# Optimization experiments

Hardware: AMD Instinct MI355X
Metric: run time of the kernel (lower is better)

## Reference

```python
import jax, jax.numpy as jnp
import numpy as np
import math

B, C, L = 8, 64, 2048
H = 4            # num_heads
CH = C // H      # head channels = 16
G = max(1, C // 16)  # GroupNorm groups = 4
EPS = 1e-5


def setup_inputs() -> dict:
    key = jax.random.key(0)
    ks = jax.random.split(key, 4)
    x = jax.random.normal(ks[0], (B, C, L), dtype=jnp.float32)
    gn_w = jnp.ones((C,), jnp.float32)
    gn_b = jnp.zeros((C,), jnp.float32)
    qkv_w = jax.random.normal(ks[1], (3 * C, C), jnp.float32) / math.sqrt(C)
    qkv_b = jnp.zeros((3 * C,), jnp.float32)
    # note: original zero-inits proj_out; we use random weights for a non-trivial baseline
    proj_w = jax.random.normal(ks[2], (C, C), jnp.float32) / math.sqrt(C)
    proj_b = jnp.zeros((C,), jnp.float32)
    return {"x": x, "gn_w": gn_w, "gn_b": gn_b, "qkv_w": qkv_w,
            "qkv_b": qkv_b, "proj_w": proj_w, "proj_b": proj_b}


def _group_norm(x, w, b):
    # x: [B, C, L], groups over channel dim
    xg = x.reshape(B, G, (C // G) * L)
    mean = jnp.mean(xg, axis=-1, keepdims=True)
    var = jnp.var(xg, axis=-1, keepdims=True)
    xn = ((xg - mean) * jax.lax.rsqrt(var + EPS)).reshape(B, C, L)
    return xn * w[None, :, None] + b[None, :, None]


def reference(x, gn_w, gn_b, qkv_w, qkv_b, proj_w, proj_b):
    xn = _group_norm(x, gn_w, gn_b)
    # conv1x1 QKV: [B, 3C, L]
    qkv = jnp.einsum('oc,bcl->bol', qkv_w, xn) + qkv_b[None, :, None]
    q, k, v = jnp.split(qkv, 3, axis=1)            # each [B, C, L]
    q = q.reshape(B * H, CH, L)
    k = k.reshape(B * H, CH, L)
    v = v.reshape(B * H, CH, L)
    scale = 1.0 / math.sqrt(math.sqrt(CH))          # double-scaled as in source
    w = jnp.einsum('bct,bcs->bts', q * scale, k * scale)  # [B*H, L, L]
    w = jax.nn.softmax(w.astype(jnp.float32), axis=-1).astype(q.dtype)
    a = jnp.einsum('bts,bcs->bct', w, v).reshape(B, C, L)
    h = jnp.einsum('oc,bcl->bol', proj_w, a) + proj_b[None, :, None]
    return x + h
```

## Files before the change

kernel.cpp:

```cpp
#include <hip/hip_runtime.h>
#include <hip/hip_bf16.h>

#define LL 2048

typedef float f32x16 __attribute__((ext_vector_type(16)));
typedef float f32x4 __attribute__((ext_vector_type(4)));
typedef short short8 __attribute__((ext_vector_type(8)));

__device__ __forceinline__ float exp2_fast(float x) {
    float r;
    asm volatile("v_exp_f32 %0, %1" : "=v"(r) : "v"(x));
    return r;
}

__device__ __forceinline__ float rcp_fast(float x) {
    float r;
    asm("v_rcp_f32 %0, %1" : "=v"(r) : "v"(x));
    return r;
}

__device__ __forceinline__ uint32_t cvtpk(float lo, float hi) {
    uint32_t r;
    asm("v_cvt_pk_bf16_f32 %0, %1, %2" : "=v"(r) : "v"(lo), "v"(hi));
    return r;
}

__device__ __forceinline__ unsigned short bf16lo(float a) {
    return (unsigned short)(cvtpk(a, a) & 0xFFFFu);
}

__device__ __forceinline__ void permswap(uint32_t& d, uint32_t& s) {
    asm("v_permlane32_swap_b32 %0, %1" : "+v"(d), "+v"(s));
}

__global__ __launch_bounds__(256) void k_gnstats(const float* __restrict__ x,
                                                 const float* __restrict__ qw,
                                                 const float* __restrict__ pw,
                                                 float* __restrict__ stats,
                                                 unsigned short* __restrict__ ones,
                                                 unsigned short* __restrict__ wqb) {
    if (blockIdx.x == 0) {
        uint4 v = make_uint4(0x3F803F80u, 0x3F803F80u, 0x3F803F80u, 0x3F803F80u);
        *(uint4*)(ones + threadIdx.x * 16)     = v;
        *(uint4*)(ones + threadIdx.x * 16 + 8) = v;
    }
    if (blockIdx.x >= 8 && blockIdx.x < 16) {
        int idx8 = (blockIdx.x - 8) * 2048 + threadIdx.x * 8;
        const float* src = (idx8 < 12288) ? qw + idx8 : pw + (idx8 - 12288);
        f32x4 a = *(const f32x4*)src;
        f32x4 c = *(const f32x4*)(src + 4);
        uint4 o = make_uint4(cvtpk(a[0], a[1]), cvtpk(a[2], a[3]),
                             cvtpk(c[0], c[1]), cvtpk(c[2], c[3]));
        *(uint4*)(wqb + idx8) = o;
    }
    int bg = blockIdx.x >> 2, part = blockIdx.x & 3;
    const f32x4* p = (const f32x4*)(x + (size_t)bg * (16 * LL)) + part * 2048;
    float s1 = 0.f, s2 = 0.f;
    for (int i = threadIdx.x; i < 2048; i += 256) {
        f32x4 v = p[i];
        s1 += v[0] + v[1] + v[2] + v[3];
        s2 += v[0] * v[0] + v[1] * v[1] + v[2] * v[2] + v[3] * v[3];
    }
#pragma unroll
    for (int off = 32; off > 0; off >>= 1) {
        s1 += __shfl_down(s1, off, 64);
        s2 += __shfl_down(s2, off, 64);
    }
    __shared__ float r1[4], r2[4];
    int lane = threadIdx.x & 63, wv = threadIdx.x >> 6;
    if (lane == 0) { r1[wv] = s1; r2[wv] = s2; }
    __syncthreads();
    if (threadIdx.x == 0) {
        stats[blockIdx.x * 2]     = r1[0] + r1[1] + r1[2] + r1[3];
        stats[blockIdx.x * 2 + 1] = r2[0] + r2[1] + r2[2] + r2[3];
    }
}

__global__ __launch_bounds__(256) void k_qkv(const float* __restrict__ x,
                                             const float* __restrict__ gnw,
                                             const float* __restrict__ gnb,
                                             const unsigned short* __restrict__ wqb,
                                             const float* __restrict__ qb,
                                             const float* __restrict__ stats,
                                             unsigned short* __restrict__ qt,
                                             unsigned short* __restrict__ kt,
                                             unsigned short* __restrict__ vb) {
    int lt = blockIdx.x;
    int b  = blockIdx.y;
    int tid = threadIdx.x;
    int l0 = lt * 64;
    __shared__ unsigned short xs[64 * 64];
    __shared__ unsigned short ws[3][64 * 64];
    __shared__ float wb[64][2];

    if (tid < 64) {
        int c = tid, g = c >> 4;
        int sb = (b * 4 + g) * 8;
        float s1 = stats[sb] + stats[sb + 2] + stats[sb + 4] + stats[sb + 6];
        float s2 = stats[sb + 1] + stats[sb + 3] + stats[sb + 5] + stats[sb + 7];
        float mean = s1 * (1.0f / 32768.0f);
        float var  = s2 * (1.0f / 32768.0f) - mean * mean;
        float rstd = rsqrtf(var + 1e-5f);
        float wgt = gnw[c] * rstd;
        wb[c][0] = wgt;
        wb[c][1] = gnb[c] - mean * wgt;
    }
#pragma unroll
    for (int ot = 0; ot < 3; ot++) {
#pragma unroll
        for (int k = 0; k < 4; k++) {
            int chunk = tid + k * 256;
            int o = chunk >> 4, c4 = chunk & 15;
            uint2 w2 = *(const uint2*)(wqb + (size_t)(ot * 64 + o) * 64 + c4 * 4);
            *(uint2*)&ws[ot][o * 64 + ((c4 * 4) ^ ((o & 7) << 3))] = w2;
        }
    }
    __syncthreads();

    {
        int cq = tid >> 4, l4 = tid & 15, c0 = cq * 4;
        f32x4 xv0 = *(const f32x4*)(x + ((size_t)b * 64 + c0)     * LL + l0 + l4 * 4);
        f32x4 xv1 = *(const f32x4*)(x + ((size_t)b * 64 + c0 + 1) * LL + l0 + l4 * 4);
        f32x4 xv2 = *(const f32x4*)(x + ((size_t)b * 64 + c0 + 2) * LL + l0 + l4 * 4);
        f32x4 xv3 = *(const f32x4*)(x + ((size_t)b * 64 + c0 + 3) * LL + l0 + l4 * 4);
        float w0 = wb[c0][0], b0 = wb[c0][1];
        float w1 = wb[c0 + 1][0], b1 = wb[c0 + 1][1];
        float w2 = wb[c0 + 2][0], b2 = wb[c0 + 2][1];
        float w3 = wb[c0 + 3][0], b3 = wb[c0 + 3][1];
#pragma unroll
        for (int j = 0; j < 4; j++) {
            int l = l4 * 4 + j;
            uint32_t lo = cvtpk(xv0[j] * w0 + b0, xv1[j] * w1 + b1);
            uint32_t hw = cvtpk(xv2[j] * w2 + b2, xv3[j] * w3 + b3);
            *(uint2*)&xs[l * 64 + (c0 ^ ((l & 7) << 3))] = make_uint2(lo, hw);
        }
    }
    __syncthreads();

    int wv_ = tid >> 6, lane = tid & 63, hi = lane >> 5, tl = lane & 31;
    int o0 = (wv_ & 1) * 32, lw = (wv_ >> 1) * 32;
    int arow = o0 + tl, brow = lw + tl;
    int t = l0 + lw + tl;

#pragma unroll
    for (int ot = 0; ot < 3; ot++) {
        f32x16 acc = {};
#pragma unroll
        for (int kk = 0; kk < 4; kk++) {
            int cb = kk * 16 + hi * 8;
            short8 af = *(const short8*)&ws[ot][arow * 64 + (cb ^ ((arow & 7) << 3))];
            short8 bf = *(const short8*)&xs[brow * 64 + (cb ^ ((brow & 7) << 3))];
            acc = __builtin_amdgcn_mfma_f32_32x32x16_bf16(af, bf, acc, 0, 0, 0);
        }
        if (ot < 2) {
            float sc = ot ? 0.72134752f : 0.5f;
            unsigned short* base = (ot ? kt : qt) + (size_t)(b * 4) * (LL * 16);
#pragma unroll
            for (int g = 0; g < 4; g++) {
                int ob = o0 + 8 * g + 4 * hi;
                float v0 = (acc[4 * g]     + qb[ot * 64 + ob])     * sc;
                float v1 = (acc[4 * g + 1] + qb[ot * 64 + ob + 1]) * sc;
                float v2 = (acc[4 * g + 2] + qb[ot * 64 + ob + 2]) * sc;
                float v3 = (acc[4 * g + 3] + qb[ot * 64 + ob + 3]) * sc;
                uint2 pkv = make_uint2(cvtpk(v0, v1), cvtpk(v2, v3));
                *(uint2*)(base + (size_t)(ob >> 4) * (LL * 16)
                          + (size_t)t * 16 + (ob & 15)) = pkv;
            }
        } else {
            unsigned short* base = vb + (size_t)(b * 4) * (16 * LL);
#pragma unroll
            for (int r = 0; r < 16; r++) {
                int o = o0 + (r & 3) + 8 * (r >> 2) + 4 * hi;
                base[(size_t)(o >> 4) * (16 * LL) + (size_t)(o & 15) * LL + t] =
                    bf16lo(acc[r] + qb[128 + o]);
            }
        }
    }
}

__global__ __launch_bounds__(256) void k_attn(const unsigned short* __restrict__ qt,
                                              const unsigned short* __restrict__ kt,
                                              const unsigned short* __restrict__ vb,
                                              unsigned short* __restrict__ abuf) {
    int wv = threadIdx.x >> 6;
    int lane = threadIdx.x & 63;
    int hi = lane >> 5, tlo = lane & 31;
    int bh = blockIdx.y;
    int t0 = blockIdx.x * 32;

    __shared__ float lds_d2[3][32][33];

    const unsigned short* qp = qt + (size_t)bh * (LL * 16);
    const unsigned short* kbase = kt + (size_t)bh * (LL * 16);
    const unsigned short* vbase = vb + (size_t)bh * (16 * LL);

    int koff = (wv * 512 + tlo) * 16 + 8 * hi;
    int voff = (tlo < 16 ? tlo * LL : (32 - bh) * 16 * LL) + wv * 512 + 8 * hi;

    short8 qf = *(const short8*)(qp + (size_t)(t0 + tlo) * 16 + 8 * hi);

    const f32x16 z = {};
    f32x16 d2 = {};

    short8 kfa = *(const short8*)&kbase[koff];
    short8 kfb = *(const short8*)&kbase[koff + 512];
    short8 vA0 = *(const short8*)&vbase[voff];
    short8 vA1 = *(const short8*)&vbase[voff + 16];
    short8 vB0 = *(const short8*)&vbase[voff + 32];
    short8 vB1 = *(const short8*)&vbase[voff + 48];
    f32x16 d1A = __builtin_amdgcn_mfma_f32_32x32x16_bf16(kfa, qf, z, 0, 0, 0);
    f32x16 d1B = __builtin_amdgcn_mfma_f32_32x32x16_bf16(kfb, qf, z, 0, 0, 0);

    int kpre = koff + 1024;
    int vpre = voff + 64;

#define SOFTMAX_PV(D1, V0, V1)                                                \
    {                                                                         \
        uint32_t pk0 = cvtpk(exp2_fast(D1[0]),  exp2_fast(D1[1]));            \
        uint32_t pk1 = cvtpk(exp2_fast(D1[2]),  exp2_fast(D1[3]));            \
        uint32_t pk2 = cvtpk(exp2_fast(D1[4]),  exp2_fast(D1[5]));            \
        uint32_t pk3 = cvtpk(exp2_fast(D1[6]),  exp2_fast(D1[7]));            \
        uint32_t pk4 = cvtpk(exp2_fast(D1[8]),  exp2_fast(D1[9]));            \
        uint32_t pk5 = cvtpk(exp2_fast(D1[10]), exp2_fast(D1[11]));           \
        uint32_t pk6 = cvtpk(exp2_fast(D1[12]), exp2_fast(D1[13]));           \
        uint32_t pk7 = cvtpk(exp2_fast(D1[14]), exp2_fast(D1[15]));           \
        permswap(pk0, pk2);                                                   \
        permswap(pk1, pk3);                                                   \
        permswap(pk4, pk6);                                                   \
        permswap(pk5, pk7);                                                   \
        union { uint32_t u[4]; short8 s; } A1_, A2_;                          \
        A1_.u[0] = pk0; A1_.u[1] = pk1; A1_.u[2] = pk2; A1_.u[3] = pk3;       \
        A2_.u[0] = pk4; A2_.u[1] = pk5; A2_.u[2] = pk6; A2_.u[3] = pk7;       \
        d2 = __builtin_amdgcn_mfma_f32_32x32x16_bf16(A1_.s, V0, d2, 0, 0, 0); \
        d2 = __builtin_amdgcn_mfma_f32_32x32x16_bf16(A2_.s, V1, d2, 0, 0, 0); \
    }

#pragma unroll 2
    for (int it = 0; it < 8; ++it) {
        kfa = *(const short8*)&kbase[kpre];
        SOFTMAX_PV(d1A, vA0, vA1)
        vA0 = *(const short8*)&vbase[vpre];
        vA1 = *(const short8*)&vbase[vpre + 16];
        d1A = __builtin_amdgcn_mfma_f32_32x32x16_bf16(kfa, qf, z, 0, 0, 0);
        kfb = *(const short8*)&kbase[kpre + 512];
        SOFTMAX_PV(d1B, vB0, vB1)
        vB0 = *(const short8*)&vbase[vpre + 32];
        vB1 = *(const short8*)&vbase[vpre + 48];
        d1B = __builtin_amdgcn_mfma_f32_32x32x16_bf16(kfb, qf, z, 0, 0, 0);
        kpre += 1024;
        vpre += 64;
    }
#undef SOFTMAX_PV

    if (wv > 0) {
        int w = wv - 1;
#pragma unroll
        for (int r = 0; r < 16; r++) {
            int row = (r & 3) + 8 * (r >> 2) + 4 * hi;
            lds_d2[w][row][tlo] = d2[r];
        }
    }
    __syncthreads();
    if (wv == 0) {
        unsigned short* op = abuf + ((size_t)bh * 16 + tlo) * LL + t0;
        float v[16];
#pragma unroll
        for (int r = 0; r < 16; r++) {
            int row = (r & 3) + 8 * (r >> 2) + 4 * hi;
            float osum = d2[r] + lds_d2[0][row][tlo]
                       + lds_d2[1][row][tlo] + lds_d2[2][row][tlo];
            float rv = rcp_fast(osum);
            float rl = __shfl_xor(rv, 16, 64);
            v[r] = osum * rl;
        }
        if (tlo < 16) {
#pragma unroll
            for (int g = 0; g < 4; g++) {
                uint2 pkv = make_uint2(cvtpk(v[4 * g], v[4 * g + 1]),
                                       cvtpk(v[4 * g + 2], v[4 * g + 3]));
                *(uint2*)(op + 8 * g + 4 * hi) = pkv;
            }
        }
    }
}

__global__ __launch_bounds__(256) void k_proj(const float* __restrict__ x,
                                              const unsigned short* __restrict__ abuf,
                                              const unsigned short* __restrict__ wpb,
                                              const float* __restrict__ pb,
                                              float* __restrict__ out) {
    int lt = blockIdx.x;
    int b  = blockIdx.y;
    int tid = threadIdx.x;
    int l0 = lt * 64;
    __shared__ unsigned short as_[64 * 64];
    __shared__ unsigned short ws[64 * 64];

    {
        int cq = tid >> 4, t4 = tid & 15, c0 = cq * 4;
        uint2 ld0 = *(const uint2*)(abuf + (size_t)(b * 64 + c0)     * LL + l0 + t4 * 4);
        uint2 ld1 = *(const uint2*)(abuf + (size_t)(b * 64 + c0 + 1) * LL + l0 + t4 * 4);
        uint2 ld2 = *(const uint2*)(abuf + (size_t)(b * 64 + c0 + 2) * LL + l0 + t4 * 4);
        uint2 ld3 = *(const uint2*)(abuf + (size_t)(b * 64 + c0 + 3) * LL + l0 + t4 * 4);
        const unsigned short* s0 = (const unsigned short*)&ld0;
        const unsigned short* s1 = (const unsigned short*)&ld1;
        const unsigned short* s2 = (const unsigned short*)&ld2;
        const unsigned short* s3 = (const unsigned short*)&ld3;
#pragma unroll
        for (int j = 0; j < 4; j++) {
            int l = t4 * 4 + j;
            uint32_t lo = (uint32_t)s0[j] | ((uint32_t)s1[j] << 16);
            uint32_t hw = (uint32_t)s2[j] | ((uint32_t)s3[j] << 16);
            *(uint2*)&as_[l * 64 + (c0 ^ ((l & 7) << 3))] = make_uint2(lo, hw);
        }
    }
#pragma unroll
    for (int k = 0; k < 4; k++) {
        int chunk = tid + k * 256;
        int o = chunk >> 4, c4 = chunk & 15;
        uint2 w2 = *(const uint2*)(wpb + (size_t)o * 64 + c4 * 4);
        *(uint2*)&ws[o * 64 + ((c4 * 4) ^ ((o & 7) << 3))] = w2;
    }
    __syncthreads();

    int wv_ = tid >> 6, lane = tid & 63, hi = lane >> 5, tl = lane & 31;
    int o0 = (wv_ & 1) * 32, lw = (wv_ >> 1) * 32;
    int arow = o0 + tl, brow = lw + tl;
    f32x16 acc = {};
#pragma unroll
    for (int kk = 0; kk < 4; kk++) {
        int cb = kk * 16 + hi * 8;
        short8 af = *(const short8*)&ws[arow * 64 + (cb ^ ((arow & 7) << 3))];
        short8 bf = *(const short8*)&as_[brow * 64 + (cb ^ ((brow & 7) << 3))];
        acc = __builtin_amdgcn_mfma_f32_32x32x16_bf16(af, bf, acc, 0, 0, 0);
    }

    int l = l0 + lw + tl;
#pragma unroll
    for (int r = 0; r < 16; r++) {
        int o = o0 + (r & 3) + 8 * (r >> 2) + 4 * hi;
        size_t idx = (size_t)(b * 64 + o) * LL + l;
        out[idx] = x[idx] + acc[r] + pb[o];
    }
}

extern "C" void kernel_launch(void* const* d_in, const int* in_sizes, int n_in,
                              void* d_out, int out_size, void* d_ws, size_t ws_size,
                              hipStream_t stream) {
    const float* x   = (const float*)d_in[0];
    const float* gnw = (const float*)d_in[1];
    const float* gnb = (const float*)d_in[2];
    const float* qw  = (const float*)d_in[3];
    const float* qb  = (const float*)d_in[4];
    const float* pw  = (const float*)d_in[5];
    const float* pb  = (const float*)d_in[6];
    float* out = (float*)d_out;

    float* wsf   = (float*)d_ws;
    float* stats = wsf;
    unsigned short* qt = (unsigned short*)(wsf + 256);
    unsigned short* kt = qt + (size_t)32 * LL * 16;
    unsigned short* vb = kt + (size_t)32 * LL * 16;
    unsigned short* ones = vb + (size_t)32 * LL * 16;
    unsigned short* abuf = ones + 4096;
    unsigned short* wqb  = abuf + (size_t)8 * 64 * LL;
    unsigned short* wpb  = wqb + 12288;

    hipLaunchKernelGGL(k_gnstats, dim3(128), dim3(256), 0, stream,
                       x, qw, pw, stats, ones, wqb);
    hipLaunchKernelGGL(k_qkv, dim3(32, 8), dim3(256), 0, stream,
                       x, gnw, gnb, wqb, qb, stats, qt, kt, vb);
    hipLaunchKernelGGL(k_attn, dim3(64, 32), dim3(256), 0, stream,
                       qt, kt, vb, abuf);
    hipLaunchKernelGGL(k_proj, dim3(32, 8), dim3(256), 0, stream,
                       x, abuf, wpb, pb, out);
}
```

Before: 110.6 us.

## Fuse output projection and residual add into attention kernel

```diff
diff --git a/kernel.cpp b/kernel.cpp
--- a/kernel.cpp
+++ b/kernel.cpp
@@ -178,24 +178,39 @@
     }
 }
 
-__global__ __launch_bounds__(256) void k_attn(const unsigned short* __restrict__ qt,
-                                              const unsigned short* __restrict__ kt,
-                                              const unsigned short* __restrict__ vb,
-                                              unsigned short* __restrict__ abuf) {
-    int wv = threadIdx.x >> 6;
-    int lane = threadIdx.x & 63;
+__global__ __launch_bounds__(1024) void k_attn(const unsigned short* __restrict__ qt,
+                                               const unsigned short* __restrict__ kt,
+                                               const unsigned short* __restrict__ vb,
+                                               const unsigned short* __restrict__ wpb,
+                                               const float* __restrict__ pb,
+                                               const float* __restrict__ x,
+                                               float* __restrict__ out) {
+    int tid = threadIdx.x;
+    int wv = tid >> 6;
+    int h  = wv >> 2;
+    int sp = wv & 3;
+    int lane = tid & 63;
     int hi = lane >> 5, tlo = lane & 31;
-    int bh = blockIdx.y;
+    int b = blockIdx.y;
+    int bh = b * 4 + h;
     int t0 = blockIdx.x * 32;
 
-    __shared__ float lds_d2[3][32][33];
+    __shared__ float lds_d2[4][3][32][33];
+    __shared__ unsigned short ostage[32 * 68];
+    __shared__ unsigned short wsh[64 * 64];
+
+    {
+        int o = tid >> 4, c4 = tid & 15;
+        uint2 w2 = *(const uint2*)(wpb + (size_t)o * 64 + c4 * 4);
+        *(uint2*)&wsh[o * 64 + ((c4 * 4) ^ ((o & 7) << 3))] = w2;
+    }
 
     const unsigned short* qp = qt + (size_t)bh * (LL * 16);
     const unsigned short* kbase = kt + (size_t)bh * (LL * 16);
     const unsigned short* vbase = vb + (size_t)bh * (16 * LL);
 
-    int koff = (wv * 512 + tlo) * 16 + 8 * hi;
-    int voff = (tlo < 16 ? tlo * LL : (32 - bh) * 16 * LL) + wv * 512 + 8 * hi;
+    int koff = (sp * 512 + tlo) * 16 + 8 * hi;
+    int voff = (tlo < 16 ? tlo * LL : (32 - bh) * 16 * LL) + sp * 512 + 8 * hi;
 
     short8 qf = *(const short8*)(qp + (size_t)(t0 + tlo) * 16 + 8 * hi);
 
@@ -252,95 +267,55 @@
     }
 #undef SOFTMAX_PV
 
-    if (wv > 0) {
-        int w = wv - 1;
+    if (sp > 0) {
+        int w = sp - 1;
 #pragma unroll
         for (int r = 0; r < 16; r++) {
             int row = (r & 3) + 8 * (r >> 2) + 4 * hi;
-            lds_d2[w][row][tlo] = d2[r];
-        }
-    }
-    __syncthreads();
-    if (wv == 0) {
-        unsigned short* op = abuf + ((size_t)bh * 16 + tlo) * LL + t0;
+            lds_d2[h][w][row][tlo] = d2[r];
+        }
+    }
+    __syncthreads();
+    if (sp == 0) {
         float v[16];
 #pragma unroll
         for (int r = 0; r < 16; r++) {
             int row = (r & 3) + 8 * (r >> 2) + 4 * hi;
-            float osum = d2[r] + lds_d2[0][row][tlo]
-                       + lds_d2[1][row][tlo] + lds_d2[2][row][tlo];
+            float osum = d2[r] + lds_d2[h][0][row][tlo]
+                       + lds_d2[h][1][row][tlo] + lds_d2[h][2][row][tlo];
             float rv = rcp_fast(osum);
             float rl = __shfl_xor(rv, 16, 64);
             v[r] = osum * rl;
         }
         if (tlo < 16) {
-#pragma unroll
-            for (int g = 0; g < 4; g++) {
-                uint2 pkv = make_uint2(cvtpk(v[4 * g], v[4 * g + 1]),
-                                       cvtpk(v[4 * g + 2], v[4 * g + 3]));
-                *(uint2*)(op + 8 * g + 4 * hi) = pkv;
+            int c = h * 16 + tlo;
+#pragma unroll
+            for (int r = 0; r < 16; r++) {
+                int row = (r & 3) + 8 * (r >> 2) + 4 * hi;
+                ostage[row * 68 + c] = bf16lo(v[r]);
             }
         }
     }
-}
-
-__global__ __launch_bounds__(256) void k_proj(const float* __restrict__ x,
-                                              const unsigned short* __restrict__ abuf,
-                                              const unsigned short* __restrict__ wpb,
-                                              const float* __restrict__ pb,
-                                              float* __restrict__ out) {
-    int lt = blockIdx.x;
-    int b  = blockIdx.y;
-    int tid = threadIdx.x;
-    int l0 = lt * 64;
-    __shared__ unsigned short as_[64 * 64];
-    __shared__ unsigned short ws[64 * 64];
-
-    {
-        int cq = tid >> 4, t4 = tid & 15, c0 = cq * 4;
-        uint2 ld0 = *(const uint2*)(abuf + (size_t)(b * 64 + c0)     * LL + l0 + t4 * 4);
-        uint2 ld1 = *(const uint2*)(abuf + (size_t)(b * 64 + c0 + 1) * LL + l0 + t4 * 4);
-        uint2 ld2 = *(const uint2*)(abuf + (size_t)(b * 64 + c0 + 2) * LL + l0 + t4 * 4);
-        uint2 ld3 = *(const uint2*)(abuf + (size_t)(b * 64 + c0 + 3) * LL + l0 + t4 * 4);
-        const unsigned short* s0 = (const unsigned short*)&ld0;
-        const unsigned short* s1 = (const unsigned short*)&ld1;
-        const unsigned short* s2 = (const unsigned short*)&ld2;
-        const unsigned short* s3 = (const unsigned short*)&ld3;
-#pragma unroll
-        for (int j = 0; j < 4; j++) {
-            int l = t4 * 4 + j;
-            uint32_t lo = (uint32_t)s0[j] | ((uint32_t)s1[j] << 16);
-            uint32_t hw = (uint32_t)s2[j] | ((uint32_t)s3[j] << 16);
-            *(uint2*)&as_[l * 64 + (c0 ^ ((l & 7) << 3))] = make_uint2(lo, hw);
-        }
-    }
-#pragma unroll
-    for (int k = 0; k < 4; k++) {
-        int chunk = tid + k * 256;
-        int o = chunk >> 4, c4 = chunk & 15;
-        uint2 w2 = *(const uint2*)(wpb + (size_t)o * 64 + c4 * 4);
-        *(uint2*)&ws[o * 64 + ((c4 * 4) ^ ((o & 7) << 3))] = w2;
-    }
-    __syncthreads();
-
-    int wv_ = tid >> 6, lane = tid & 63, hi = lane >> 5, tl = lane & 31;
-    int o0 = (wv_ & 1) * 32, lw = (wv_ >> 1) * 32;
-    int arow = o0 + tl, brow = lw + tl;
-    f32x16 acc = {};
-#pragma unroll
-    for (int kk = 0; kk < 4; kk++) {
-        int cb = kk * 16 + hi * 8;
-        short8 af = *(const short8*)&ws[arow * 64 + (cb ^ ((arow & 7) << 3))];
-        short8 bf = *(const short8*)&as_[brow * 64 + (cb ^ ((brow & 7) << 3))];
-        acc = __builtin_amdgcn_mfma_f32_32x32x16_bf16(af, bf, acc, 0, 0, 0);
-    }
-
-    int l = l0 + lw + tl;
-#pragma unroll
-    for (int r = 0; r < 16; r++) {
-        int o = o0 + (r & 3) + 8 * (r >> 2) + 4 * hi;
-        size_t idx = (size_t)(b * 64 + o) * LL + l;
-        out[idx] = x[idx] + acc[r] + pb[o];
+    __syncthreads();
+    if (wv == 1 || wv == 5) {
+        int o0 = (wv == 5) ? 32 : 0;
+        int arow = o0 + tlo;
+        f32x16 acc = {};
+#pragma unroll
+        for (int kk = 0; kk < 4; kk++) {
+            int cb = kk * 16 + hi * 8;
+            short8 af = *(const short8*)&wsh[arow * 64 + (cb ^ ((arow & 7) << 3))];
+            union { uint2 u2[2]; short8 s; } B;
+            B.u2[0] = *(const uint2*)&ostage[tlo * 68 + cb];
+            B.u2[1] = *(const uint2*)&ostage[tlo * 68 + cb + 4];
+            acc = __builtin_amdgcn_mfma_f32_32x32x16_bf16(af, B.s, acc, 0, 0, 0);
+        }
+#pragma unroll
+        for (int r = 0; r < 16; r++) {
+            int o = o0 + (r & 3) + 8 * (r >> 2) + 4 * hi;
+            size_t idx = (size_t)(b * 64 + o) * LL + t0 + tlo;
+            out[idx] = x[idx] + acc[r] + pb[o];
+        }
     }
 }
 
@@ -362,16 +337,13 @@
     unsigned short* kt = qt + (size_t)32 * LL * 16;
     unsigned short* vb = kt + (size_t)32 * LL * 16;
     unsigned short* ones = vb + (size_t)32 * LL * 16;
-    unsigned short* abuf = ones + 4096;
-    unsigned short* wqb  = abuf + (size_t)8 * 64 * LL;
+    unsigned short* wqb  = ones + 4096;
     unsigned short* wpb  = wqb + 12288;
 
     hipLaunchKernelGGL(k_gnstats, dim3(128), dim3(256), 0, stream,
                        x, qw, pw, stats, ones, wqb);
     hipLaunchKernelGGL(k_qkv, dim3(32, 8), dim3(256), 0, stream,
                        x, gnw, gnb, wqb, qb, stats, qt, kt, vb);
-    hipLaunchKernelGGL(k_attn, dim3(64, 32), dim3(256), 0, stream,
-                       qt, kt, vb, abuf);
-    hipLaunchKernelGGL(k_proj, dim3(32, 8), dim3(256), 0, stream,
-                       x, abuf, wpb, pb, out);
-}
+    hipLaunchKernelGGL(k_attn, dim3(64, 8), dim3(1024), 0, stream,
+                       qt, kt, vb, wpb, pb, x, out);
+}
```

After: 105.9 us. -4.2%, faster.
